# Optimization experiments

Hardware: AMD Instinct MI355X
Metric: run time of the kernel (lower is better)

Reference implementation:

```python
import jax, jax.numpy as jnp
import numpy as np

N, E, T, R, L = 100000, 800000, 2, 4, 2
DIN, H, C, DOUT = 16, 256, 128, 4
EPS = 1e-5


def hetero_linear(x, node_type, W, b):
    # y[i] = x[i] @ W[node_type[i]] + b[node_type[i]]; small fixed T loop
    out = jnp.zeros((x.shape[0], W.shape[-1]), x.dtype)
    for t in range(W.shape[0]):
        out = out + jnp.where((node_type == t)[:, None], x @ W[t] + b[t], jnp.zeros((), x.dtype))
    return out


def hetero_bn(x, node_type, gamma, beta):
    # per-node-type batch norm (training-mode statistics, biased variance)
    T_ = gamma.shape[0]
    cnt = jax.ops.segment_sum(jnp.ones((x.shape[0],), x.dtype), node_type, num_segments=T_)
    cnt = jnp.maximum(cnt, 1.0)[:, None]
    mean = jax.ops.segment_sum(x, node_type, num_segments=T_) / cnt
    var = jax.ops.segment_sum(x * x, node_type, num_segments=T_) / cnt - mean * mean
    inv = jax.lax.rsqrt(var + EPS)
    return (x - mean[node_type]) * inv[node_type] * gamma[node_type] + beta[node_type]


def rgcn_conv(x, edge_index, edge_type, W, root, bias):
    # RGCNConv with sum aggregation: out_i = x_i @ root + b + sum_{(j->i), r} x_j @ W_r
    src, dst = edge_index[0], edge_index[1]
    hs = jnp.einsum('nd,rdf->rnf', x, W)          # [R, N, C]
    msg = hs[edge_type, src]                       # [E, C] per-edge relation-transformed source feats
    agg = jax.ops.segment_sum(msg, dst, num_segments=x.shape[0])
    return agg + x @ root + bias


def setup_inputs() -> dict:
    key = jax.random.key(0)
    ks = iter(jax.random.split(key, 40))

    def w(shape, fan_in):
        return jax.random.normal(next(ks), shape, jnp.float32) / np.float32(np.sqrt(fan_in))

    inp = {}
    inp['x'] = jax.random.normal(next(ks), (N, DIN), jnp.float32)
    inp['edge_index'] = jax.random.randint(next(ks), (2, E), 0, N)
    inp['node_type'] = jax.random.randint(next(ks), (N,), 0, T)
    inp['edge_type'] = jax.random.randint(next(ks), (E,), 0, R)
    inp['ri_w0'] = w((T, DIN, H), DIN); inp['ri_b0'] = jnp.zeros((T, H))
    inp['ri_g0'] = jnp.ones((T, H)); inp['ri_be0'] = jnp.zeros((T, H))
    inp['ri_w1'] = w((T, H, C), H); inp['ri_b1'] = jnp.zeros((T, C))
    inp['cn_g'] = jnp.ones((L, T, C)); inp['cn_b'] = jnp.zeros((L, T, C))
    inp['rg_w'] = w((L, R, C, C), C); inp['rg_root'] = w((L, C, C), C); inp['rg_bias'] = jnp.zeros((L, C))
    inp['mn_g'] = jnp.ones((L, T, C)); inp['mn_b'] = jnp.zeros((L, T, C))
    inp['mw0'] = w((L, T, C, H), C); inp['mb0'] = jnp.zeros((L, T, H))
    inp['mg0'] = jnp.ones((L, T, H)); inp['mbe0'] = jnp.zeros((L, T, H))
    inp['mw1'] = w((L, T, H, C), H); inp['mb1'] = jnp.zeros((L, T, C))
    inp['ro_w0'] = w((T, C, H), C); inp['ro_b0'] = jnp.zeros((T, H))
    inp['ro_g0'] = jnp.ones((T, H)); inp['ro_be0'] = jnp.zeros((T, H))
    inp['ro_w1'] = w((T, H, DOUT), H); inp['ro_b1'] = jnp.zeros((T, DOUT))
    return inp


def reference(x, edge_index, node_type, edge_type,
              ri_w0, ri_b0, ri_g0, ri_be0, ri_w1, ri_b1,
              cn_g, cn_b, rg_w, rg_root, rg_bias,
              mn_g, mn_b, mw0, mb0, mg0, mbe0, mw1, mb1,
              ro_w0, ro_b0, ro_g0, ro_be0, ro_w1, ro_b1):
    act = jax.nn.leaky_relu  # negative_slope 0.01, as nn.LeakyReLU default
    # readin MLP (plain_last)
    h = hetero_linear(x, node_type, ri_w0, ri_b0)
    h = act(hetero_bn(h, node_type, ri_g0, ri_be0))
    h = hetero_linear(h, node_type, ri_w1, ri_b1)
    # RES+ blocks: Norm -> Act -> Conv -> +res, Norm -> Act -> MLP -> +res (dropout=0)
    for l in range(rg_w.shape[0]):
        y = act(hetero_bn(h, node_type, cn_g[l], cn_b[l]))
        h = h + rgcn_conv(y, edge_index, edge_type, rg_w[l], rg_root[l], rg_bias[l])
        y = act(hetero_bn(h, node_type, mn_g[l], mn_b[l]))
        y = hetero_linear(y, node_type, mw0[l], mb0[l])
        y = act(hetero_bn(y, node_type, mg0[l], mbe0[l]))
        y = hetero_linear(y, node_type, mw1[l], mb1[l])
        h = h + y
    # readout MLP (plain_last)
    h = hetero_linear(h, node_type, ro_w0, ro_b0)
    h = act(hetero_bn(h, node_type, ro_g0, ro_be0))
    return hetero_linear(h, node_type, ro_w1, ro_b1)
```

## Files before the change

kernel.cpp:

```cpp
#include <hip/hip_runtime.h>

#define TT 2
#define RR 4
#define LL 2
#define DIN 16
#define HH 256
#define CC 128
#define DOUT 4
#define EPS 1e-5f
#define NB 32
#define NBG 16

typedef float v4f __attribute__((ext_vector_type(4)));
typedef short bf16x8 __attribute__((ext_vector_type(8)));

__device__ __forceinline__ ushort f2bf(float x) {
    uint u = __float_as_uint(x);
    return (ushort)((u + 0x7fffu + ((u >> 16) & 1u)) >> 16);
}
__device__ __forceinline__ float bf2f(ushort h) { return __uint_as_float(((uint)h) << 16); }
__device__ __forceinline__ int swc(int c) { return c ^ ((c >> 3) & 7); }
__device__ __forceinline__ uint pack2(float x, float y) {
    return (uint)f2bf(x) | ((uint)f2bf(y) << 16);
}

__global__ __launch_bounds__(1024) void k_scan1(const int* __restrict__ in, int* __restrict__ out,
                                                int* __restrict__ part, int n) {
    __shared__ int sm[1024];
    const int tid = threadIdx.x;
    const int i = blockIdx.x * 1024 + tid;
    const int v = (i < n) ? in[i] : 0;
    sm[tid] = v;
    __syncthreads();
    for (int off = 1; off < 1024; off <<= 1) {
        const int u = (tid >= off) ? sm[tid - off] : 0;
        __syncthreads();
        sm[tid] += u;
        __syncthreads();
    }
    if (i < n) out[i] = sm[tid] - v;
    if (tid == 1023) part[blockIdx.x] = sm[1023];
}

__global__ __launch_bounds__(1024) void k_scan2(int* __restrict__ part, int nb) {
    __shared__ int sm[1024];
    const int tid = threadIdx.x;
    const int v = (tid < nb) ? part[tid] : 0;
    sm[tid] = v;
    __syncthreads();
    for (int off = 1; off < 1024; off <<= 1) {
        const int u = (tid >= off) ? sm[tid - off] : 0;
        __syncthreads();
        sm[tid] += u;
        __syncthreads();
    }
    if (tid < nb) part[tid] = sm[tid] - v;
    if (tid == nb - 1) part[nb] = sm[tid];
}

__global__ __launch_bounds__(1024) void k_scan3(int* __restrict__ arr, const int* __restrict__ part,
                                                int n, int nb) {
    const int i = blockIdx.x * 1024 + threadIdx.x;
    if (i < n) arr[i] += part[i >> 10];
    else if (i == n) arr[n] = part[nb];
}

__global__ void k_meta(const int* __restrict__ pscan, int* __restrict__ typeStart, int n) {
    const int c1 = pscan[n];
    typeStart[0] = 0; typeStart[1] = n - c1; typeStart[2] = n;
}

__global__ __launch_bounds__(256) void k_build_perm(const int* __restrict__ nt, const int* __restrict__ pscan,
                                                    const int* __restrict__ typeStart, int* __restrict__ perm,
                                                    int* __restrict__ inv, int n) {
    const int i = blockIdx.x * 256 + threadIdx.x;
    if (i >= n) return;
    const int s1 = pscan[i];
    const int pos = nt[i] ? (typeStart[1] + s1) : (i - s1);
    perm[pos] = i;
    inv[i] = pos;
}

__global__ __launch_bounds__(256) void k_deg2(const int* __restrict__ dstv, const int* __restrict__ et,
                                              const int* __restrict__ inv, int* __restrict__ rowp2, int nE) {
    const int e = blockIdx.x * 256 + threadIdx.x;
    if (e < nE) atomicAdd(&rowp2[inv[dstv[e]] * 4 + et[e]], 1);
}

__global__ __launch_bounds__(256) void k_fill2(const int* __restrict__ srcv, const int* __restrict__ dstv,
                                               const int* __restrict__ et, const int* __restrict__ inv,
                                               int* __restrict__ cur, int* __restrict__ csr, int nE) {
    const int e = blockIdx.x * 256 + threadIdx.x;
    if (e < nE) {
        const int pos = atomicAdd(&cur[inv[dstv[e]] * 4 + et[e]], 1);
        csr[pos] = inv[srcv[e]];
    }
}

__global__ __launch_bounds__(256) void k_pack(const float* __restrict__ src, ushort* __restrict__ dst,
                                              int K, int N, long long total) {
    for (long long idx = (long long)blockIdx.x * 256 + threadIdx.x; idx < total;
         idx += (long long)gridDim.x * 256) {
        const long long kn = (long long)K * N;
        const int mat = (int)(idx / kn);
        const int rem = (int)(idx - mat * kn);
        const int k = rem / N, col = rem % N;
        dst[((size_t)mat * (K / 8) + (k >> 3)) * N * 8 + (size_t)col * 8 + (k & 7)] = f2bf(src[idx]);
    }
}

__global__ __launch_bounds__(256) void k_pack_conv(const float* __restrict__ rgw, const float* __restrict__ root,
                                                   ushort* __restrict__ dst) {
    const int idx = blockIdx.x * 256 + threadIdx.x;
    if (idx >= 640 * 128) return;
    const int k = idx >> 7, col = idx & 127;
    const float v = (k < 512) ? rgw[(((k >> 7) * CC) + (k & 127)) * CC + col]
                              : root[(size_t)(k - 512) * CC + col];
    dst[((size_t)(k >> 3) * CC + col) * 8 + (k & 7)] = f2bf(v);
}

__global__ __launch_bounds__(512) void k_coef(const float* __restrict__ stat, const int* __restrict__ typeStart,
                                              const float* __restrict__ g, const float* __restrict__ be,
                                              float* __restrict__ scale, float* __restrict__ shift, int F) {
    const int tid = threadIdx.x;
    if (tid >= TT * F) return;
    const int t = tid / F;
    float s = 0.f, q = 0.f;
    for (int b = 0; b < NB; ++b) {
        s += stat[(size_t)b * 1024 + tid];
        q += stat[(size_t)b * 1024 + 512 + tid];
    }
    const float cnt = fmaxf((float)(typeStart[t + 1] - typeStart[t]), 1.f);
    const float mean = s / cnt;
    const float var = q / cnt - mean * mean;
    const float sc = g[tid] * rsqrtf(var + EPS);
    scale[tid] = sc;
    shift[tid] = be[tid] - mean * sc;
}

__global__ __launch_bounds__(256) void k_gram(const float* __restrict__ x, const int* __restrict__ perm,
                                              const int* __restrict__ typeStart, float* __restrict__ gram) {
    __shared__ float Xs[256][17];
    const int tid = threadIdx.x;
    const int t = blockIdx.y;
    const int rbeg = typeStart[t], rend = typeStart[t + 1];
    const int r0 = rbeg + blockIdx.x * 1024;
    if (r0 >= rend) return;
    const int i = tid >> 4, j = tid & 15;
    float acc = 0.f, sacc = 0.f;
    for (int rr = 0; rr < 4; ++rr) {
        const int gr = r0 + rr * 256 + tid;
        v4f x0 = 0.f, x1 = 0.f, x2 = 0.f, x3 = 0.f;
        if (gr < rend) {
            const float* xr = x + (size_t)perm[gr] * DIN;
            x0 = *(const v4f*)xr; x1 = *(const v4f*)(xr + 4);
            x2 = *(const v4f*)(xr + 8); x3 = *(const v4f*)(xr + 12);
        }
        __syncthreads();
#pragma unroll
        for (int e = 0; e < 4; ++e) { Xs[tid][e] = x0[e]; Xs[tid][4 + e] = x1[e];
                                      Xs[tid][8 + e] = x2[e]; Xs[tid][12 + e] = x3[e]; }
        __syncthreads();
        for (int r = 0; r < 256; ++r) acc += Xs[r][i] * Xs[r][j];
        if (tid < 16)
            for (int r = 0; r < 256; ++r) sacc += Xs[r][tid];
        __syncthreads();
    }
    float* gb = gram + ((size_t)t * NBG + (blockIdx.x & (NBG - 1))) * 272;
    atomicAdd(&gb[tid], acc);
    if (tid < 16) atomicAdd(&gb[256 + tid], sacc);
}

__global__ __launch_bounds__(512) void k_ri_coef(const float* __restrict__ gram, const int* __restrict__ typeStart,
                                                 const float* __restrict__ ri_w0, const float* __restrict__ ri_b0,
                                                 const float* __restrict__ g, const float* __restrict__ be,
                                                 float* __restrict__ w0eff, float* __restrict__ b0eff) {
    __shared__ float G[2][272];
    const int tid = threadIdx.x;
    for (int idx = tid; idx < 2 * 272; idx += 512) {
        const int tt = idx / 272, k = idx % 272;
        float s = 0.f;
        for (int b = 0; b < NBG; ++b) s += gram[((size_t)tt * NBG + b) * 272 + k];
        G[tt][k] = s;
    }
    __syncthreads();
    const int t = tid >> 8, c = tid & 255;
    float wv[16];
#pragma unroll
    for (int k = 0; k < 16; ++k) wv[k] = ri_w0[((size_t)t * 16 + k) * HH + c];
    const float b = ri_b0[t * HH + c];
    const float cnt = fmaxf((float)(typeStart[t + 1] - typeStart[t]), 1.f);
    float sw = 0.f;
#pragma unroll
    for (int k = 0; k < 16; ++k) sw += G[t][256 + k] * wv[k];
    const float mean = (sw + cnt * b) / cnt;
    float e2 = 0.f;
#pragma unroll
    for (int i = 0; i < 16; ++i) {
        const float wi = wv[i];
#pragma unroll
        for (int j = 0; j < 16; ++j) e2 += wi * wv[j] * G[t][i * 16 + j];
    }
    e2 = (e2 + 2.f * b * sw + cnt * b * b) / cnt;
    const float var = e2 - mean * mean;
    const float sc = g[t * HH + c] * rsqrtf(var + EPS);
    const float sf = be[t * HH + c] - mean * sc;
    b0eff[t * HH + c] = b * sc + sf;
#pragma unroll
    for (int k = 0; k < 16; ++k) w0eff[((size_t)t * 16 + k) * HH + c] = wv[k] * sc;
}

__global__ __launch_bounds__(256) void k_readin(const float* __restrict__ x, const int* __restrict__ perm,
                                                const int* __restrict__ typeStart,
                                                const float* __restrict__ w0eff, const float* __restrict__ b0eff,
                                                const ushort* __restrict__ Wp, const float* __restrict__ b1,
                                                float* __restrict__ h, ushort* __restrict__ h16,
                                                float* __restrict__ stat) {
    __shared__ float Xs[128][17];
    __shared__ float W0s[16][256];
    __shared__ float b0s[256];
    __shared__ ushort As[128][40];
    __shared__ ushort Ws[4][128][8];

    const int tid = threadIdx.x;
    const int lane = tid & 63;
    const int wid = tid >> 6;
    const int woffm = (wid >> 1) * 64, woffn = (wid & 1) * 64;
    const int t = blockIdx.y;
    const int rbeg = typeStart[t], rend = typeStart[t + 1];
    const int r0 = rbeg + blockIdx.x * 128;
    if (r0 >= rend) return;

    for (int idx = tid; idx < 16 * 256; idx += 256) W0s[idx >> 8][idx & 255] = w0eff[(size_t)t * 4096 + idx];
    if (tid < 256) b0s[tid] = b0eff[t * 256 + tid];

    const int srow = tid >> 1, half = tid & 1;
    const int sgr = r0 + srow;
    const bool svalid = sgr < rend;
    {
        v4f x0 = 0.f, x1 = 0.f;
        if (svalid) {
            const float* xr = x + (size_t)perm[sgr] * DIN + half * 8;
            x0 = *(const v4f*)xr; x1 = *(const v4f*)(xr + 4);
        }
#pragma unroll
        for (int e = 0; e < 4; ++e) { Xs[srow][half * 8 + e] = x0[e]; Xs[srow][half * 8 + 4 + e] = x1[e]; }
    }
    __syncthreads();
    float xr[16];
#pragma unroll
    for (int k = 0; k < 16; ++k) xr[k] = Xs[srow][k];

    v4f acc[4][4];
#pragma unroll
    for (int mt = 0; mt < 4; ++mt)
#pragma unroll
        for (int nt = 0; nt < 4; ++nt) acc[mt][nt] = (v4f){0.f, 0.f, 0.f, 0.f};

    const size_t wmat = (size_t)t * 256 * 128;
    const int wcp = tid & 63;

    for (int kt = 0; kt < 8; ++kt) {
        const int k0 = kt * 32;
        ushort hA[16];
#pragma unroll
        for (int c2 = 0; c2 < 16; ++c2) {
            const int col = k0 + half * 16 + c2;
            float d = b0s[col];
#pragma unroll
            for (int k = 0; k < 16; ++k) d = fmaf(xr[k], W0s[k][col], d);
            d = fmaxf(d, 0.01f * d);
            hA[c2] = f2bf(d);
        }
        const ushort* wsrc = Wp + wmat + ((size_t)(k0 / 8 + wid) * 128) * 8 + (size_t)wcp * 16;
        const uint4 w0 = *(const uint4*)wsrc;
        const uint4 w1 = *(const uint4*)(wsrc + 8);
        __syncthreads();
        *(uint4*)&As[srow][half * 16] = *(uint4*)&hA[0];
        *(uint4*)&As[srow][half * 16 + 8] = *(uint4*)&hA[8];
        *(uint4*)&Ws[wid][swc(wcp * 2)][0] = w0;
        *(uint4*)&Ws[wid][swc(wcp * 2 + 1)][0] = w1;
        __syncthreads();
        const int afr = lane & 15;
        const int akg = (lane >> 4) * 8;
        bf16x8 aF[4], wf[4];
#pragma unroll
        for (int mt = 0; mt < 4; ++mt) aF[mt] = *(const bf16x8*)&As[woffm + mt * 16 + afr][akg];
#pragma unroll
        for (int nt = 0; nt < 4; ++nt) wf[nt] = *(const bf16x8*)&Ws[lane >> 4][swc(woffn + nt * 16 + afr)][0];
#pragma unroll
        for (int mt = 0; mt < 4; ++mt)
#pragma unroll
            for (int nt = 0; nt < 4; ++nt)
                acc[mt][nt] = __builtin_amdgcn_mfma_f32_16x16x32_bf16(aF[mt], wf[nt], acc[mt][nt], 0, 0, 0);
    }

    float bv[4];
#pragma unroll
    for (int nt = 0; nt < 4; ++nt) bv[nt] = b1[t * 128 + woffn + nt * 16 + (lane & 15)];
    float cs[4] = {0.f, 0.f, 0.f, 0.f}, cq[4] = {0.f, 0.f, 0.f, 0.f};
#pragma unroll
    for (int mt = 0; mt < 4; ++mt) {
        const int grow = r0 + woffm + mt * 16 + (lane >> 4) * 4;
#pragma unroll
        for (int nt = 0; nt < 4; ++nt) {
            const int gcol = woffn + nt * 16 + (lane & 15);
#pragma unroll
            for (int rg = 0; rg < 4; ++rg) {
                const int gr = grow + rg;
                if (gr < rend) {
                    const float v = acc[mt][nt][rg] + bv[nt];
                    const size_t o = (size_t)gr * 128 + gcol;
                    h[o] = v;
                    h16[o] = f2bf(v);
                    cs[nt] += v; cq[nt] += v * v;
                }
            }
        }
    }
    float* sb = stat + (size_t)(blockIdx.x & (NB - 1)) * 1024;
#pragma unroll
    for (int nt = 0; nt < 4; ++nt) {
        float s = cs[nt], q = cq[nt];
        s += __shfl_xor(s, 16); q += __shfl_xor(q, 16);
        s += __shfl_xor(s, 32); q += __shfl_xor(q, 32);
        if (lane < 16) {
            const int col = t * 128 + woffn + nt * 16 + lane;
            atomicAdd(&sb[col], s);
            atomicAdd(&sb[512 + col], q);
        }
    }
}

__global__ __launch_bounds__(256) void k_agg4(const ushort* __restrict__ h16, const int* __restrict__ rowp2,
                                              const int* __restrict__ csr, const float* __restrict__ scale,
                                              const float* __restrict__ shift, const int* __restrict__ typeStart,
                                              ushort* __restrict__ buf, int q0, int q1) {
    const int wid = threadIdx.x >> 6, lane = threadIdx.x & 63;
    const int i = q0 + blockIdx.x * 4 + wid;
    if (i >= q1) return;
    const int c = 2 * lane;
    const int c0 = typeStart[1];
    const float2 sa0 = *(const float2*)(scale + c);
    const float2 sb0 = *(const float2*)(shift + c);
    const float2 sa1 = *(const float2*)(scale + CC + c);
    const float2 sb1 = *(const float2*)(shift + CC + c);
    const uint* h32 = (const uint*)h16;
    float2 a0 = {0.f, 0.f}, a1 = {0.f, 0.f}, a2 = {0.f, 0.f}, a3 = {0.f, 0.f};
    const int e0 = rowp2[4 * i], b1 = rowp2[4 * i + 1], b2 = rowp2[4 * i + 2],
              b3 = rowp2[4 * i + 3], e1 = rowp2[4 * i + 4];
    for (int e = e0; e < e1; e += 64) {
        const int cnt = min(64, e1 - e);
        int pk = (lane < cnt) ? csr[e + lane] : 0;
        for (int j = 0; j < cnt; ++j) {
            const int s = __shfl(pk, j);
            const int idx = e + j;
            const bool tb = s >= c0;
            const uint u = h32[(size_t)s * 64 + lane];
            float vx = fmaf(bf2f((ushort)(u & 0xffff)), tb ? sa1.x : sa0.x, tb ? sb1.x : sb0.x);
            float vy = fmaf(bf2f((ushort)(u >> 16)), tb ? sa1.y : sa0.y, tb ? sb1.y : sb0.y);
            vx = fmaxf(vx, 0.01f * vx);
            vy = fmaxf(vy, 0.01f * vy);
            if (idx < b1)      { a0.x += vx; a0.y += vy; }
            else if (idx < b2) { a1.x += vx; a1.y += vy; }
            else if (idx < b3) { a2.x += vx; a2.y += vy; }
            else               { a3.x += vx; a3.y += vy; }
        }
    }
    const bool td = i >= c0;
    const uint hu = h32[(size_t)i * 64 + lane];
    float yx = fmaf(bf2f((ushort)(hu & 0xffff)), td ? sa1.x : sa0.x, td ? sb1.x : sb0.x);
    float yy = fmaf(bf2f((ushort)(hu >> 16)), td ? sa1.y : sa0.y, td ? sb1.y : sb0.y);
    yx = fmaxf(yx, 0.01f * yx);
    yy = fmaxf(yy, 0.01f * yy);
    uint* brow = (uint*)buf + (size_t)(i - q0) * 320;
    brow[0 * 64 + lane] = pack2(a0.x, a0.y);
    brow[1 * 64 + lane] = pack2(a1.x, a1.y);
    brow[2 * 64 + lane] = pack2(a2.x, a2.y);
    brow[3 * 64 + lane] = pack2(a3.x, a3.y);
    brow[256 + lane] = pack2(yx, yy);
}

__global__ __launch_bounds__(256) void k_add_stats(float* __restrict__ h, ushort* __restrict__ h16,
                                                   const float* __restrict__ tc,
                                                   const int* __restrict__ typeStart, float* __restrict__ stat,
                                                   int n) {
    __shared__ float red[256 * 17];
    const int tid = threadIdx.x;
    const int c = tid & 31;
    const int rs = tid >> 5;
    const int c0 = typeStart[1];
    const int i0 = blockIdx.x * 256;
    const int i1 = min(n, i0 + 256);
    v4f s0 = 0.f, q0 = 0.f, s1 = 0.f, q1 = 0.f;
    for (int i = i0 + rs; i < i1; i += 8) {
        v4f a = *(const v4f*)(h + (size_t)i * CC + 4 * c);
        a += *(const v4f*)(tc + (size_t)i * CC + 4 * c);
        *(v4f*)(h + (size_t)i * CC + 4 * c) = a;
        ushort4 hh = make_ushort4(f2bf(a[0]), f2bf(a[1]), f2bf(a[2]), f2bf(a[3]));
        *(ushort4*)(h16 + (size_t)i * CC + 4 * c) = hh;
        if (i < c0) { s0 += a; q0 += a * a; }
        else        { s1 += a; q1 += a * a; }
    }
#pragma unroll
    for (int j = 0; j < 4; ++j) {
        red[tid * 17 + j] = s0[j];
        red[tid * 17 + 4 + j] = q0[j];
        red[tid * 17 + 8 + j] = s1[j];
        red[tid * 17 + 12 + j] = q1[j];
    }
    __syncthreads();
    float* sb = stat + (size_t)(blockIdx.x & (NB - 1)) * 1024;
    for (int o = tid; o < 512; o += 256) {
        const int col = o & 127, m = (o >> 7) & 1, t = (o >> 8) & 1;
        const int reg = t * 8 + m * 4 + (col & 3);
        float v = 0.f;
#pragma unroll
        for (int r = 0; r < 8; ++r) v += red[((col >> 2) + 32 * r) * 17 + reg];
        atomicAdd(&sb[(m ? 512 : 0) + t * CC + col], v);
    }
}

template <int K, int OUTW, bool TYPED, bool WHET, bool XBF, bool BNIN, bool BHET, bool STATS, int OUTMODE>
__global__ __launch_bounds__(256) void k_mf(
    const float* __restrict__ Xf, const ushort* __restrict__ Xb,
    const ushort* __restrict__ Wp, const float* __restrict__ Bb,
    const float* __restrict__ scale, const float* __restrict__ shift,
    const int* __restrict__ typeStart, float* __restrict__ Y,
    ushort* __restrict__ Y16, float* __restrict__ stat,
    int rbase, int rbeg_u, int rend_u) {
    __shared__ ushort As[128][40];
    __shared__ ushort Ws[4][128][8];
    __shared__ float csh[BNIN ? K : 1];
    __shared__ float cfh[BNIN ? K : 1];

    const int tid = threadIdx.x;
    const int lane = tid & 63;
    const int wid = tid >> 6;
    const int woffm = (wid >> 1) * 64, woffn = (wid & 1) * 64;

    int t = 0, rbeg = rbeg_u, rend = rend_u;
    if constexpr (TYPED) { t = blockIdx.y; rbeg = typeStart[t]; rend = typeStart[t + 1]; }
    const int r0 = rbeg + blockIdx.x * 128;
    if (r0 >= rend) return;
    const int zoff = (OUTW == 256) ? blockIdx.z * 128 : 0;

    if constexpr (BNIN) {
        for (int k = tid; k < K; k += 256) { csh[k] = scale[t * K + k]; cfh[k] = shift[t * K + k]; }
        __syncthreads();
    }

    const int srow = tid >> 1, scg = (tid & 1) * 16;
    const int sgr = r0 + srow;
    const bool svalid = sgr < rend;
    const int wcp = tid & 63;

    v4f acc[4][4];
#pragma unroll
    for (int mt = 0; mt < 4; ++mt)
#pragma unroll
        for (int nt = 0; nt < 4; ++nt) acc[mt][nt] = (v4f){0.f, 0.f, 0.f, 0.f};

    const size_t wmat = (size_t)(WHET ? t : 0) * K * OUTW;

    for (int kt = 0; kt < K / 32; ++kt) {
        const int k0 = kt * 32;
        uint uu[8];
        if constexpr (XBF) {
            uint4 a0 = make_uint4(0, 0, 0, 0), a1 = make_uint4(0, 0, 0, 0);
            if (svalid) {
                const ushort* xs = Xb + (size_t)(sgr - rbase) * K + k0 + scg;
                a0 = *(const uint4*)xs;
                a1 = *(const uint4*)(xs + 8);
            }
            uu[0] = a0.x; uu[1] = a0.y; uu[2] = a0.z; uu[3] = a0.w;
            uu[4] = a1.x; uu[5] = a1.y; uu[6] = a1.z; uu[7] = a1.w;
            if constexpr (BNIN) {
#pragma unroll
                for (int e = 0; e < 8; ++e) {
                    const int k = k0 + scg + 2 * e;
                    float f0 = fmaf(bf2f((ushort)(uu[e] & 0xffff)), csh[k], cfh[k]);
                    float f1 = fmaf(bf2f((ushort)(uu[e] >> 16)), csh[k + 1], cfh[k + 1]);
                    f0 = fmaxf(f0, 0.01f * f0);
                    f1 = fmaxf(f1, 0.01f * f1);
                    uu[e] = pack2(f0, f1);
                }
            }
        } else {
            float fv[16];
            {
                v4f av0 = 0.f, av1 = 0.f, av2 = 0.f, av3 = 0.f;
                if (svalid) {
                    const float* xs = Xf + (size_t)sgr * K + k0 + scg;
                    av0 = *(const v4f*)xs; av1 = *(const v4f*)(xs + 4);
                    av2 = *(const v4f*)(xs + 8); av3 = *(const v4f*)(xs + 12);
                }
#pragma unroll
                for (int e = 0; e < 4; ++e) { fv[e] = av0[e]; fv[4 + e] = av1[e];
                                              fv[8 + e] = av2[e]; fv[12 + e] = av3[e]; }
            }
            if constexpr (BNIN) {
#pragma unroll
                for (int e = 0; e < 16; ++e) {
                    const int k = k0 + scg + e;
                    float vv = fmaf(fv[e], csh[k], cfh[k]);
                    fv[e] = fmaxf(vv, 0.01f * vv);
                }
            }
#pragma unroll
            for (int e = 0; e < 8; ++e) uu[e] = pack2(fv[2 * e], fv[2 * e + 1]);
        }
        const ushort* wsrc = Wp + wmat + ((size_t)(k0 / 8 + wid) * OUTW + zoff) * 8 + (size_t)wcp * 16;
        const uint4 w0 = *(const uint4*)wsrc;
        const uint4 w1 = *(const uint4*)(wsrc + 8);

        __syncthreads();
        *(uint4*)&As[srow][scg] = make_uint4(uu[0], uu[1], uu[2], uu[3]);
        *(uint4*)&As[srow][scg + 8] = make_uint4(uu[4], uu[5], uu[6], uu[7]);
        *(uint4*)&Ws[wid][swc(wcp * 2)][0] = w0;
        *(uint4*)&Ws[wid][swc(wcp * 2 + 1)][0] = w1;
        __syncthreads();

        const int afr = lane & 15;
        const int akg = (lane >> 4) * 8;
        bf16x8 aF[4], wf[4];
#pragma unroll
        for (int mt = 0; mt < 4; ++mt) aF[mt] = *(const bf16x8*)&As[woffm + mt * 16 + afr][akg];
#pragma unroll
        for (int nt = 0; nt < 4; ++nt) wf[nt] = *(const bf16x8*)&Ws[lane >> 4][swc(woffn + nt * 16 + afr)][0];
#pragma unroll
        for (int mt = 0; mt < 4; ++mt)
#pragma unroll
            for (int nt = 0; nt < 4; ++nt)
                acc[mt][nt] = __builtin_amdgcn_mfma_f32_16x16x32_bf16(aF[mt], wf[nt], acc[mt][nt], 0, 0, 0);
    }

    const float* BbT = Bb + (BHET ? (size_t)t * OUTW : 0);
    float bv[4];
#pragma unroll
    for (int nt = 0; nt < 4; ++nt) bv[nt] = BbT[zoff + woffn + nt * 16 + (lane & 15)];
    const int c0 = (STATS && !TYPED) ? typeStart[1] : 0;
    float cs0[4] = {0.f, 0.f, 0.f, 0.f}, cq0[4] = {0.f, 0.f, 0.f, 0.f};
    float cs1[4] = {0.f, 0.f, 0.f, 0.f}, cq1[4] = {0.f, 0.f, 0.f, 0.f};
#pragma unroll
    for (int mt = 0; mt < 4; ++mt) {
        const int grow = r0 + woffm + mt * 16 + (lane >> 4) * 4;
#pragma unroll
        for (int nt = 0; nt < 4; ++nt) {
            const int gcol = zoff + woffn + nt * 16 + (lane & 15);
#pragma unroll
            for (int rg = 0; rg < 4; ++rg) {
                const int gr = grow + rg;
                if (gr < rend) {
                    float v = acc[mt][nt][rg] + bv[nt];
                    const size_t o = (size_t)gr * OUTW + gcol;
                    if constexpr (OUTMODE == 0) Y[o] = v;
                    if constexpr (OUTMODE == 1) Y16[o] = f2bf(v);
                    if constexpr (OUTMODE == 2) {
                        const float hv = Y[o] + v;
                        Y[o] = hv;
                        Y16[o] = f2bf(hv);
                        v = hv;
                    }
                    if constexpr (STATS) {
                        if (TYPED || gr < c0) { cs0[nt] += v; cq0[nt] += v * v; }
                        else                  { cs1[nt] += v; cq1[nt] += v * v; }
                    }
                }
            }
        }
    }
    if constexpr (STATS) {
        float* sb = stat + (size_t)(blockIdx.x & (NB - 1)) * 1024;
#pragma unroll
        for (int nt = 0; nt < 4; ++nt) {
            float s = cs0[nt], q = cq0[nt];
            s += __shfl_xor(s, 16); q += __shfl_xor(q, 16);
            s += __shfl_xor(s, 32); q += __shfl_xor(q, 32);
            if (lane < 16) {
                const int col = t * OUTW + zoff + woffn + nt * 16 + lane;
                atomicAdd(&sb[col], s);
                atomicAdd(&sb[512 + col], q);
            }
            if constexpr (!TYPED) {
                float s1 = cs1[nt], q1 = cq1[nt];
                s1 += __shfl_xor(s1, 16); q1 += __shfl_xor(q1, 16);
                s1 += __shfl_xor(s1, 32); q1 += __shfl_xor(q1, 32);
                if (lane < 16) {
                    const int col = OUTW + zoff + woffn + nt * 16 + lane;
                    atomicAdd(&sb[col], s1);
                    atomicAdd(&sb[512 + col], q1);
                }
            }
        }
    }
}

__global__ __launch_bounds__(256) void k_ro1(const ushort* __restrict__ A256b, const int* __restrict__ perm,
                                             const int* __restrict__ typeStart, const float* __restrict__ ro_w1,
                                             const float* __restrict__ ro_b1, const float* __restrict__ scale,
                                             const float* __restrict__ shift, float* __restrict__ out, int n) {
    __shared__ float W1s[2][256][4];
    __shared__ float scs[512];
    __shared__ float sfs[512];
    const int tid = threadIdx.x;
    for (int idx = tid; idx < 2048; idx += 256) {
        const int t = idx >> 10, rem = idx & 1023;
        W1s[t][rem >> 2][rem & 3] = ro_w1[idx];
    }
    for (int idx = tid; idx < 512; idx += 256) { scs[idx] = scale[idx]; sfs[idx] = shift[idx]; }
    __syncthreads();
    const int trow = tid >> 2, sub = tid & 3;
    const int gr = blockIdx.x * 64 + trow;
    if (gr >= n) return;
    const int c0 = typeStart[1];
    const int t = (gr >= c0) ? 1 : 0;
    v4f acc = 0.f;
    const ushort* ar = A256b + (size_t)gr * 256 + sub * 64;
#pragma unroll
    for (int q = 0; q < 8; ++q) {
        const uint4 u = *(const uint4*)(ar + q * 8);
        const uint uw[4] = {u.x, u.y, u.z, u.w};
#pragma unroll
        for (int e = 0; e < 4; ++e) {
#pragma unroll
            for (int hl = 0; hl < 2; ++hl) {
                const int col = sub * 64 + q * 8 + 2 * e + hl;
                const float v = bf2f((ushort)(hl ? (uw[e] >> 16) : (uw[e] & 0xffff)));
                float vv = fmaf(v, scs[t * 256 + col], sfs[t * 256 + col]);
                vv = fmaxf(vv, 0.01f * vv);
                acc += vv * *(const v4f*)&W1s[t][col][0];
            }
        }
    }
#pragma unroll
    for (int e = 0; e < 4; ++e) { acc[e] += __shfl_xor(acc[e], 1); acc[e] += __shfl_xor(acc[e], 2); }
    if (sub == 0) {
        acc += *(const v4f*)(ro_b1 + t * 4);
        *(v4f*)(out + (size_t)perm[gr] * 4) = acc;
    }
}

extern "C" void kernel_launch(void* const* d_in, const int* in_sizes, int n_in,
                              void* d_out, int out_size, void* d_ws, size_t ws_size,
                              hipStream_t stream) {
    const float* x = (const float*)d_in[0];
    const int* ei = (const int*)d_in[1];
    const int* nt = (const int*)d_in[2];
    const int* et = (const int*)d_in[3];
    const float* ri_w0 = (const float*)d_in[4];
    const float* ri_b0 = (const float*)d_in[5];
    const float* ri_g0 = (const float*)d_in[6];
    const float* ri_be0 = (const float*)d_in[7];
    const float* ri_w1 = (const float*)d_in[8];
    const float* ri_b1 = (const float*)d_in[9];
    const float* cn_g = (const float*)d_in[10];
    const float* cn_b = (const float*)d_in[11];
    const float* rg_w = (const float*)d_in[12];
    const float* rg_root = (const float*)d_in[13];
    const float* rg_bias = (const float*)d_in[14];
    const float* mn_g = (const float*)d_in[15];
    const float* mn_b = (const float*)d_in[16];
    const float* mw0 = (const float*)d_in[17];
    const float* mb0 = (const float*)d_in[18];
    const float* mg0 = (const float*)d_in[19];
    const float* mbe0 = (const float*)d_in[20];
    const float* mw1 = (const float*)d_in[21];
    const float* mb1 = (const float*)d_in[22];
    const float* ro_w0 = (const float*)d_in[23];
    const float* ro_b0 = (const float*)d_in[24];
    const float* ro_g0 = (const float*)d_in[25];
    const float* ro_be0 = (const float*)d_in[26];
    const float* ro_w1 = (const float*)d_in[27];
    const float* ro_b1 = (const float*)d_in[28];

    const int n = in_sizes[2];
    const int nE = in_sizes[3];
    const int* srcv = ei;
    const int* dstv = ei + nE;

    char* w = (char*)d_ws;
    size_t off = 0;
    auto alloc = [&](size_t bytes) -> char* {
        char* p = w + off;
        off = (off + bytes + 255) & ~(size_t)255;
        return p;
    };
    float* h = (float*)alloc((size_t)n * CC * sizeof(float));
    ushort* h16 = (ushort*)alloc((size_t)n * CC * sizeof(ushort));
    int* csr = (int*)alloc((size_t)nE * sizeof(int));
    int* rowp2 = (int*)alloc(((size_t)4 * n + 1) * sizeof(int));
    int* perm = (int*)alloc((size_t)n * sizeof(int));
    int* inv = (int*)alloc((size_t)n * sizeof(int));
    int* pscan = (int*)alloc((size_t)(n + 1) * sizeof(int));
    int* part = (int*)alloc(2052 * sizeof(int));
    int* typeStart = (int*)alloc(64);
    float* statbuf = (float*)alloc((size_t)9 * NB * 1024 * sizeof(float));
    float* gram = (float*)alloc((size_t)2 * NBG * 272 * sizeof(float));
    float* scale = (float*)alloc(512 * sizeof(float));
    float* shift = (float*)alloc(512 * sizeof(float));
    float* w0eff = (float*)alloc((size_t)2 * 16 * 256 * sizeof(float));
    float* b0eff = (float*)alloc(512 * sizeof(float));
    ushort* pw_ri1 = (ushort*)alloc(65536 * 2);
    ushort* pw_mw0 = (ushort*)alloc(131072 * 2);
    ushort* pw_mw1 = (ushort*)alloc(131072 * 2);
    ushort* pw_ro0 = (ushort*)alloc(65536 * 2);
    ushort* pw_conv = (ushort*)alloc(163840 * 2);
    char* region2 = alloc((size_t)n * 512);
    if (ws_size < off) return;

    ushort* A256b = (ushort*)region2;
    float* tconv = (float*)region2;
    int* cur2 = (int*)region2;
    float* out = (float*)d_out;

    ushort* buf = (ushort*)(w + off);
    const size_t bufBytes = (ws_size > off) ? (ws_size - off) : 0;
    const long long chkcap = (long long)(bufBytes / 1280);
    if (chkcap < 1024) return;
    int nchunk, CHK;
    if (chkcap >= n) { nchunk = 1; CHK = n; }
    else { nchunk = (int)((n + chkcap - 1) / chkcap); CHK = (n + nchunk - 1) / nchunk; }

    auto SS = [&](int slot) { return statbuf + (size_t)slot * NB * 1024; };

    const int gE = (nE + 255) / 256;
    const int gN = (n + 255) / 256;
    const int nb = (n + 1023) / 1024;
    const int m4 = 4 * n;
    const int nb2 = (m4 + 1023) / 1024;
    const int gmx = (n + 127) / 128;

    k_pack<<<128, 256, 0, stream>>>(ri_w1, pw_ri1, 256, 128, 2LL * 256 * 128);
    k_pack<<<256, 256, 0, stream>>>(mw0, pw_mw0, 128, 256, 4LL * 128 * 256);
    k_pack<<<256, 256, 0, stream>>>(mw1, pw_mw1, 256, 128, 4LL * 256 * 128);
    k_pack<<<128, 256, 0, stream>>>(ro_w0, pw_ro0, 128, 256, 2LL * 128 * 256);
    for (int l = 0; l < LL; ++l)
        k_pack_conv<<<320, 256, 0, stream>>>(rg_w + (size_t)l * RR * CC * CC,
                                             rg_root + (size_t)l * CC * CC,
                                             pw_conv + (size_t)l * 640 * 128);

    hipMemsetAsync(statbuf, 0, (size_t)9 * NB * 1024 * sizeof(float), stream);
    hipMemsetAsync(gram, 0, (size_t)2 * NBG * 272 * sizeof(float), stream);
    k_scan1<<<nb, 1024, 0, stream>>>(nt, pscan, part, n);
    k_scan2<<<1, 1024, 0, stream>>>(part, nb);
    k_scan3<<<(n + 1024) / 1024, 1024, 0, stream>>>(pscan, part, n, nb);
    k_meta<<<1, 1, 0, stream>>>(pscan, typeStart, n);
    k_build_perm<<<gN, 256, 0, stream>>>(nt, pscan, typeStart, perm, inv, n);
    hipMemsetAsync(rowp2, 0, ((size_t)m4 + 1) * sizeof(int), stream);
    k_deg2<<<gE, 256, 0, stream>>>(dstv, et, inv, rowp2, nE);
    k_scan1<<<nb2, 1024, 0, stream>>>(rowp2, rowp2, part, m4);
    k_scan2<<<1, 1024, 0, stream>>>(part, nb2);
    k_scan3<<<(m4 + 1024) / 1024, 1024, 0, stream>>>(rowp2, part, m4, nb2);
    hipMemcpyAsync(cur2, rowp2, (size_t)m4 * sizeof(int), hipMemcpyDeviceToDevice, stream);
    k_fill2<<<gE, 256, 0, stream>>>(srcv, dstv, et, inv, cur2, csr, nE);

    k_gram<<<dim3((n + 1023) / 1024, 2), 256, 0, stream>>>(x, perm, typeStart, gram);
    k_ri_coef<<<1, 512, 0, stream>>>(gram, typeStart, ri_w0, ri_b0, ri_g0, ri_be0, w0eff, b0eff);
    k_readin<<<dim3(gmx, 2), 256, 0, stream>>>(x, perm, typeStart, w0eff, b0eff, pw_ri1, ri_b1,
                                               h, h16, SS(1));

    for (int l = 0; l < LL; ++l) {
        const int s_cn = l ? 4 : 1, s_mn = l ? 5 : 2, s_mg = l ? 6 : 3, s_nx = l ? 7 : 4;
        k_coef<<<1, 512, 0, stream>>>(SS(s_cn), typeStart, cn_g + (size_t)l * TT * CC,
                                      cn_b + (size_t)l * TT * CC, scale, shift, CC);
        const ushort* wconv = pw_conv + (size_t)l * 640 * 128;
        if (nchunk == 1) {
            k_agg4<<<(n + 3) / 4, 256, 0, stream>>>(h16, rowp2, csr, scale, shift, typeStart, buf, 0, n);
            k_mf<640, 128, false, false, true, false, false, true, 2><<<gmx, 256, 0, stream>>>(
                nullptr, buf, wconv, rg_bias + (size_t)l * CC, nullptr, nullptr, typeStart,
                h, h16, SS(s_mn), 0, 0, n);
        } else {
            for (int q0 = 0; q0 < n; q0 += CHK) {
                const int q1 = min(n, q0 + CHK);
                k_agg4<<<(q1 - q0 + 3) / 4, 256, 0, stream>>>(h16, rowp2, csr, scale, shift,
                                                              typeStart, buf, q0, q1);
                k_mf<640, 128, false, false, true, false, false, false, 0>
                    <<<(q1 - q0 + 127) / 128, 256, 0, stream>>>(
                        nullptr, buf, wconv, rg_bias + (size_t)l * CC, nullptr, nullptr, typeStart,
                        tconv, nullptr, nullptr, q0, q0, q1);
            }
            k_add_stats<<<(n + 255) / 256, 256, 0, stream>>>(h, h16, tconv, typeStart, SS(s_mn), n);
        }

        k_coef<<<1, 512, 0, stream>>>(SS(s_mn), typeStart, mn_g + (size_t)l * TT * CC,
                                      mn_b + (size_t)l * TT * CC, scale, shift, CC);
        k_mf<128, 256, true, true, false, true, true, true, 1><<<dim3(gmx, 2, 2), 256, 0, stream>>>(
            h, nullptr, pw_mw0 + (size_t)l * 2 * 128 * 256, mb0 + (size_t)l * TT * HH,
            scale, shift, typeStart, nullptr, A256b, SS(s_mg), 0, 0, n);
        k_coef<<<1, 512, 0, stream>>>(SS(s_mg), typeStart, mg0 + (size_t)l * TT * HH,
                                      mbe0 + (size_t)l * TT * HH, scale, shift, HH);
        if (l == 0)
            k_mf<256, 128, true, true, true, true, true, true, 2><<<dim3(gmx, 2, 1), 256, 0, stream>>>(
                nullptr, A256b, pw_mw1 + (size_t)l * 2 * 256 * 128, mb1 + (size_t)l * TT * CC,
                scale, shift, typeStart, h, h16, SS(s_nx), 0, 0, n);
        else
            k_mf<256, 128, true, true, true, true, true, false, 2><<<dim3(gmx, 2, 1), 256, 0, stream>>>(
                nullptr, A256b, pw_mw1 + (size_t)l * 2 * 256 * 128, mb1 + (size_t)l * TT * CC,
                scale, shift, typeStart, h, h16, nullptr, 0, 0, n);
    }

    k_mf<128, 256, true, true, false, false, true, true, 1><<<dim3(gmx, 2, 2), 256, 0, stream>>>(
        h, nullptr, pw_ro0, ro_b0, nullptr, nullptr, typeStart, nullptr, A256b, SS(8), 0, 0, n);
    k_coef<<<1, 512, 0, stream>>>(SS(8), typeStart, ro_g0, ro_be0, scale, shift, HH);
    k_ro1<<<(n + 63) / 64, 256, 0, stream>>>(A256b, perm, typeStart, ro_w1, ro_b1, scale, shift, out, n);
}
```

Measured before the change: 839.3 us.

## Precompute BN+act once, gather bf16 activations, merge setup launches, read h16 in MLPs

Adds a k_bnact pass that applies the per-type batch norm and LeakyReLU to h once and writes a bf16 y16, so k_agg4 only gathers and sums instead of normalising every gathered edge row. The conv GEMM now reads the root input directly from y16 through a new CROOT path, which shrinks the aggregation buffer from 640 to 512 columns per row. It always uses the chunked path with stats fused in. The MLP and readout GEMMs now read bf16 h16 instead of fp32 h. Setup is also consolidated: pack kernels are merged, k_meta is folded into scan3, the memcpy is replaced by a dual write, and the two memsets are combined. Risks include an extra full pass over h and lower input precision for the MLP GEMMs.

After: 801.6 us. -4.5%, faster.

```diff
diff --git a/kernel.cpp b/kernel.cpp
--- a/kernel.cpp
+++ b/kernel.cpp
@@ -59,15 +59,18 @@
 }
 
 __global__ __launch_bounds__(1024) void k_scan3(int* __restrict__ arr, const int* __restrict__ part,
-                                                int n, int nb) {
+                                                int n, int nb, int* __restrict__ typeStart,
+                                                int* __restrict__ out2) {
     const int i = blockIdx.x * 1024 + threadIdx.x;
-    if (i < n) arr[i] += part[i >> 10];
-    else if (i == n) arr[n] = part[nb];
-}
-
-__global__ void k_meta(const int* __restrict__ pscan, int* __restrict__ typeStart, int n) {
-    const int c1 = pscan[n];
-    typeStart[0] = 0; typeStart[1] = n - c1; typeStart[2] = n;
+    if (i < n) {
+        const int v = arr[i] + part[i >> 10];
+        arr[i] = v;
+        if (out2) out2[i] = v;
+    } else if (i == n) {
+        const int total = part[nb];
+        arr[n] = total;
+        if (typeStart) { typeStart[0] = 0; typeStart[1] = n - total; typeStart[2] = n; }
+    }
 }
 
 __global__ __launch_bounds__(256) void k_build_perm(const int* __restrict__ nt, const int* __restrict__ pscan,
@@ -97,22 +100,34 @@
     }
 }
 
-__global__ __launch_bounds__(256) void k_pack(const float* __restrict__ src, ushort* __restrict__ dst,
-                                              int K, int N, long long total) {
-    for (long long idx = (long long)blockIdx.x * 256 + threadIdx.x; idx < total;
+__global__ __launch_bounds__(256) void k_packall(const float* __restrict__ ri_w1, const float* __restrict__ mw0,
+                                                 const float* __restrict__ mw1, const float* __restrict__ ro_w0,
+                                                 ushort* __restrict__ p_ri1, ushort* __restrict__ p_mw0,
+                                                 ushort* __restrict__ p_mw1, ushort* __restrict__ p_ro0) {
+    for (long long idx = (long long)blockIdx.x * 256 + threadIdx.x; idx < 393216;
          idx += (long long)gridDim.x * 256) {
-        const long long kn = (long long)K * N;
-        const int mat = (int)(idx / kn);
-        const int rem = (int)(idx - mat * kn);
+        const float* src; ushort* dst; int K, N; long long lo;
+        if (idx < 65536)       { src = ri_w1; dst = p_ri1; K = 256; N = 128; lo = idx; }
+        else if (idx < 196608) { src = mw0;   dst = p_mw0; K = 128; N = 256; lo = idx - 65536; }
+        else if (idx < 327680) { src = mw1;   dst = p_mw1; K = 256; N = 128; lo = idx - 196608; }
+        else                   { src = ro_w0; dst = p_ro0; K = 128; N = 256; lo = idx - 327680; }
+        const int kn = K * N;
+        const int mat = (int)(lo / kn);
+        const int rem = (int)(lo - (long long)mat * kn);
         const int k = rem / N, col = rem % N;
-        dst[((size_t)mat * (K / 8) + (k >> 3)) * N * 8 + (size_t)col * 8 + (k & 7)] = f2bf(src[idx]);
-    }
-}
-
-__global__ __launch_bounds__(256) void k_pack_conv(const float* __restrict__ rgw, const float* __restrict__ root,
-                                                   ushort* __restrict__ dst) {
+        dst[((size_t)mat * (K / 8) + (k >> 3)) * N * 8 + (size_t)col * 8 + (k & 7)] = f2bf(src[lo]);
+    }
+}
+
+__global__ __launch_bounds__(256) void k_pack_conv(const float* __restrict__ rgw_all,
+                                                   const float* __restrict__ root_all,
+                                                   ushort* __restrict__ dst_all) {
     const int idx = blockIdx.x * 256 + threadIdx.x;
     if (idx >= 640 * 128) return;
+    const int l = blockIdx.y;
+    const float* rgw = rgw_all + (size_t)l * RR * CC * CC;
+    const float* root = root_all + (size_t)l * CC * CC;
+    ushort* dst = dst_all + (size_t)l * 640 * 128;
     const int k = idx >> 7, col = idx & 127;
     const float v = (k < 512) ? rgw[(((k >> 7) * CC) + (k & 127)) * CC + col]
                               : root[(size_t)(k - 512) * CC + col];
@@ -136,6 +151,61 @@
     const float sc = g[tid] * rsqrtf(var + EPS);
     scale[tid] = sc;
     shift[tid] = be[tid] - mean * sc;
+}
+
+__global__ __launch_bounds__(256) void k_bnact(const float* __restrict__ h, const float* __restrict__ scale,
+                                               const float* __restrict__ shift, const int* __restrict__ typeStart,
+                                               ushort* __restrict__ y16, int n) {
+    const int c0 = typeStart[1];
+    const long long total = (long long)n * 32;
+    for (long long idx = (long long)blockIdx.x * 256 + threadIdx.x; idx < total;
+         idx += (long long)gridDim.x * 256) {
+        const int i = (int)(idx >> 5), cq = (int)(idx & 31);
+        const int t = (i >= c0) ? 1 : 0;
+        const v4f v = *(const v4f*)(h + (size_t)i * CC + cq * 4);
+        const v4f sc = *(const v4f*)(scale + t * CC + cq * 4);
+        const v4f sf = *(const v4f*)(shift + t * CC + cq * 4);
+        float o[4];
+#pragma unroll
+        for (int j = 0; j < 4; ++j) {
+            const float vv = fmaf(v[j], sc[j], sf[j]);
+            o[j] = fmaxf(vv, 0.01f * vv);
+        }
+        uint2 p = make_uint2(pack2(o[0], o[1]), pack2(o[2], o[3]));
+        *(uint2*)((uint*)y16 + (size_t)i * 64 + cq * 2) = p;
+    }
+}
+
+__global__ __launch_bounds__(256) void k_agg4(const ushort* __restrict__ y16, const int* __restrict__ rowp2,
+                                              const int* __restrict__ csr, ushort* __restrict__ buf,
+                                              int q0, int q1) {
+    const int wid = threadIdx.x >> 6, lane = threadIdx.x & 63;
+    const int i = q0 + blockIdx.x * 4 + wid;
+    if (i >= q1) return;
+    const uint* y32 = (const uint*)y16;
+    float2 a0 = {0.f, 0.f}, a1 = {0.f, 0.f}, a2 = {0.f, 0.f}, a3 = {0.f, 0.f};
+    const int e0 = rowp2[4 * i], b1 = rowp2[4 * i + 1], b2 = rowp2[4 * i + 2],
+              b3 = rowp2[4 * i + 3], e1 = rowp2[4 * i + 4];
+    for (int e = e0; e < e1; e += 64) {
+        const int cnt = min(64, e1 - e);
+        int pk = (lane < cnt) ? csr[e + lane] : 0;
+        for (int j = 0; j < cnt; ++j) {
+            const int s = __shfl(pk, j);
+            const uint u = y32[(size_t)s * 64 + lane];
+            const float vx = bf2f((ushort)(u & 0xffff));
+            const float vy = bf2f((ushort)(u >> 16));
+            const int idx = e + j;
+            if (idx < b1)      { a0.x += vx; a0.y += vy; }
+            else if (idx < b2) { a1.x += vx; a1.y += vy; }
+            else if (idx < b3) { a2.x += vx; a2.y += vy; }
+            else               { a3.x += vx; a3.y += vy; }
+        }
+    }
+    uint* brow = (uint*)buf + (size_t)(i - q0) * 256;
+    __builtin_nontemporal_store(pack2(a0.x, a0.y), brow + 0 * 64 + lane);
+    __builtin_nontemporal_store(pack2(a1.x, a1.y), brow + 1 * 64 + lane);
+    __builtin_nontemporal_store(pack2(a2.x, a2.y), brow + 2 * 64 + lane);
+    __builtin_nontemporal_store(pack2(a3.x, a3.y), brow + 3 * 64 + lane);
 }
 
 __global__ __launch_bounds__(256) void k_gram(const float* __restrict__ x, const int* __restrict__ perm,
@@ -332,98 +402,10 @@
     }
 }
 
-__global__ __launch_bounds__(256) void k_agg4(const ushort* __restrict__ h16, const int* __restrict__ rowp2,
-                                              const int* __restrict__ csr, const float* __restrict__ scale,
-                                              const float* __restrict__ shift, const int* __restrict__ typeStart,
-                                              ushort* __restrict__ buf, int q0, int q1) {
-    const int wid = threadIdx.x >> 6, lane = threadIdx.x & 63;
-    const int i = q0 + blockIdx.x * 4 + wid;
-    if (i >= q1) return;
-    const int c = 2 * lane;
-    const int c0 = typeStart[1];
-    const float2 sa0 = *(const float2*)(scale + c);
-    const float2 sb0 = *(const float2*)(shift + c);
-    const float2 sa1 = *(const float2*)(scale + CC + c);
-    const float2 sb1 = *(const float2*)(shift + CC + c);
-    const uint* h32 = (const uint*)h16;
-    float2 a0 = {0.f, 0.f}, a1 = {0.f, 0.f}, a2 = {0.f, 0.f}, a3 = {0.f, 0.f};
-    const int e0 = rowp2[4 * i], b1 = rowp2[4 * i + 1], b2 = rowp2[4 * i + 2],
-              b3 = rowp2[4 * i + 3], e1 = rowp2[4 * i + 4];
-    for (int e = e0; e < e1; e += 64) {
-        const int cnt = min(64, e1 - e);
-        int pk = (lane < cnt) ? csr[e + lane] : 0;
-        for (int j = 0; j < cnt; ++j) {
-            const int s = __shfl(pk, j);
-            const int idx = e + j;
-            const bool tb = s >= c0;
-            const uint u = h32[(size_t)s * 64 + lane];
-            float vx = fmaf(bf2f((ushort)(u & 0xffff)), tb ? sa1.x : sa0.x, tb ? sb1.x : sb0.x);
-            float vy = fmaf(bf2f((ushort)(u >> 16)), tb ? sa1.y : sa0.y, tb ? sb1.y : sb0.y);
-            vx = fmaxf(vx, 0.01f * vx);
-            vy = fmaxf(vy, 0.01f * vy);
-            if (idx < b1)      { a0.x += vx; a0.y += vy; }
-            else if (idx < b2) { a1.x += vx; a1.y += vy; }
-            else if (idx < b3) { a2.x += vx; a2.y += vy; }
-            else               { a3.x += vx; a3.y += vy; }
-        }
-    }
-    const bool td = i >= c0;
-    const uint hu = h32[(size_t)i * 64 + lane];
-    float yx = fmaf(bf2f((ushort)(hu & 0xffff)), td ? sa1.x : sa0.x, td ? sb1.x : sb0.x);
-    float yy = fmaf(bf2f((ushort)(hu >> 16)), td ? sa1.y : sa0.y, td ? sb1.y : sb0.y);
-    yx = fmaxf(yx, 0.01f * yx);
-    yy = fmaxf(yy, 0.01f * yy);
-    uint* brow = (uint*)buf + (size_t)(i - q0) * 320;
-    brow[0 * 64 + lane] = pack2(a0.x, a0.y);
-    brow[1 * 64 + lane] = pack2(a1.x, a1.y);
-    brow[2 * 64 + lane] = pack2(a2.x, a2.y);
-    brow[3 * 64 + lane] = pack2(a3.x, a3.y);
-    brow[256 + lane] = pack2(yx, yy);
-}
-
-__global__ __launch_bounds__(256) void k_add_stats(float* __restrict__ h, ushort* __restrict__ h16,
-                                                   const float* __restrict__ tc,
-                                                   const int* __restrict__ typeStart, float* __restrict__ stat,
-                                                   int n) {
-    __shared__ float red[256 * 17];
-    const int tid = threadIdx.x;
-    const int c = tid & 31;
-    const int rs = tid >> 5;
-    const int c0 = typeStart[1];
-    const int i0 = blockIdx.x * 256;
-    const int i1 = min(n, i0 + 256);
-    v4f s0 = 0.f, q0 = 0.f, s1 = 0.f, q1 = 0.f;
-    for (int i = i0 + rs; i < i1; i += 8) {
-        v4f a = *(const v4f*)(h + (size_t)i * CC + 4 * c);
-        a += *(const v4f*)(tc + (size_t)i * CC + 4 * c);
-        *(v4f*)(h + (size_t)i * CC + 4 * c) = a;
-        ushort4 hh = make_ushort4(f2bf(a[0]), f2bf(a[1]), f2bf(a[2]), f2bf(a[3]));
-        *(ushort4*)(h16 + (size_t)i * CC + 4 * c) = hh;
-        if (i < c0) { s0 += a; q0 += a * a; }
-        else        { s1 += a; q1 += a * a; }
-    }
-#pragma unroll
-    for (int j = 0; j < 4; ++j) {
-        red[tid * 17 + j] = s0[j];
-        red[tid * 17 + 4 + j] = q0[j];
-        red[tid * 17 + 8 + j] = s1[j];
-        red[tid * 17 + 12 + j] = q1[j];
-    }
-    __syncthreads();
-    float* sb = stat + (size_t)(blockIdx.x & (NB - 1)) * 1024;
-    for (int o = tid; o < 512; o += 256) {
-        const int col = o & 127, m = (o >> 7) & 1, t = (o >> 8) & 1;
-        const int reg = t * 8 + m * 4 + (col & 3);
-        float v = 0.f;
-#pragma unroll
-        for (int r = 0; r < 8; ++r) v += red[((col >> 2) + 32 * r) * 17 + reg];
-        atomicAdd(&sb[(m ? 512 : 0) + t * CC + col], v);
-    }
-}
-
-template <int K, int OUTW, bool TYPED, bool WHET, bool XBF, bool BNIN, bool BHET, bool STATS, int OUTMODE>
+template <int K, int OUTW, bool TYPED, bool WHET, bool XBF, bool CROOT, bool BNIN,
+          bool BHET, bool STATS, int OUTMODE>
 __global__ __launch_bounds__(256) void k_mf(
-    const float* __restrict__ Xf, const ushort* __restrict__ Xb,
+    const float* __restrict__ Xf, const ushort* __restrict__ Xb, const ushort* __restrict__ Xb2,
     const ushort* __restrict__ Wp, const float* __restrict__ Bb,
     const float* __restrict__ scale, const float* __restrict__ shift,
     const int* __restrict__ typeStart, float* __restrict__ Y,
@@ -434,6 +416,8 @@
     __shared__ float csh[BNIN ? K : 1];
     __shared__ float cfh[BNIN ? K : 1];
 
+    constexpr int XSTR = CROOT ? 512 : K;
+
     const int tid = threadIdx.x;
     const int lane = tid & 63;
     const int wid = tid >> 6;
@@ -467,9 +451,15 @@
         const int k0 = kt * 32;
         uint uu[8];
         if constexpr (XBF) {
+            const ushort* xs;
+            if constexpr (CROOT) {
+                xs = (k0 >= 512) ? (Xb2 + (size_t)sgr * 128 + (k0 - 512) + scg)
+                                 : (Xb + (size_t)(sgr - rbase) * XSTR + k0 + scg);
+            } else {
+                xs = Xb + (size_t)(sgr - rbase) * XSTR + k0 + scg;
+            }
             uint4 a0 = make_uint4(0, 0, 0, 0), a1 = make_uint4(0, 0, 0, 0);
             if (svalid) {
-                const ushort* xs = Xb + (size_t)(sgr - rbase) * K + k0 + scg;
                 a0 = *(const uint4*)xs;
                 a1 = *(const uint4*)(xs + 8);
             }
@@ -690,13 +680,13 @@
     ushort* h16 = (ushort*)alloc((size_t)n * CC * sizeof(ushort));
     int* csr = (int*)alloc((size_t)nE * sizeof(int));
     int* rowp2 = (int*)alloc(((size_t)4 * n + 1) * sizeof(int));
+    int* cur2 = (int*)alloc((size_t)4 * n * sizeof(int));
     int* perm = (int*)alloc((size_t)n * sizeof(int));
     int* inv = (int*)alloc((size_t)n * sizeof(int));
     int* pscan = (int*)alloc((size_t)(n + 1) * sizeof(int));
     int* part = (int*)alloc(2052 * sizeof(int));
     int* typeStart = (int*)alloc(64);
-    float* statbuf = (float*)alloc((size_t)9 * NB * 1024 * sizeof(float));
-    float* gram = (float*)alloc((size_t)2 * NBG * 272 * sizeof(float));
+    float* statgram = (float*)alloc(((size_t)9 * NB * 1024 + 2 * NBG * 272) * sizeof(float));
     float* scale = (float*)alloc(512 * sizeof(float));
     float* shift = (float*)alloc(512 * sizeof(float));
     float* w0eff = (float*)alloc((size_t)2 * 16 * 256 * sizeof(float));
@@ -709,14 +699,15 @@
     char* region2 = alloc((size_t)n * 512);
     if (ws_size < off) return;
 
+    float* statbuf = statgram;
+    float* gram = statgram + (size_t)9 * NB * 1024;
     ushort* A256b = (ushort*)region2;
-    float* tconv = (float*)region2;
-    int* cur2 = (int*)region2;
+    ushort* y16 = (ushort*)region2;
     float* out = (float*)d_out;
 
     ushort* buf = (ushort*)(w + off);
     const size_t bufBytes = (ws_size > off) ? (ws_size - off) : 0;
-    const long long chkcap = (long long)(bufBytes / 1280);
+    const long long chkcap = (long long)(bufBytes / 1024);
     if (chkcap < 1024) return;
     int nchunk, CHK;
     if (chkcap >= n) { nchunk = 1; CHK = n; }
@@ -731,28 +722,19 @@
     const int nb2 = (m4 + 1023) / 1024;
     const int gmx = (n + 127) / 128;
 
-    k_pack<<<128, 256, 0, stream>>>(ri_w1, pw_ri1, 256, 128, 2LL * 256 * 128);
-    k_pack<<<256, 256, 0, stream>>>(mw0, pw_mw0, 128, 256, 4LL * 128 * 256);
-    k_pack<<<256, 256, 0, stream>>>(mw1, pw_mw1, 256, 128, 4LL * 256 * 128);
-    k_pack<<<128, 256, 0, stream>>>(ro_w0, pw_ro0, 128, 256, 2LL * 128 * 256);
-    for (int l = 0; l < LL; ++l)
-        k_pack_conv<<<320, 256, 0, stream>>>(rg_w + (size_t)l * RR * CC * CC,
-                                             rg_root + (size_t)l * CC * CC,
-                                             pw_conv + (size_t)l * 640 * 128);
-
-    hipMemsetAsync(statbuf, 0, (size_t)9 * NB * 1024 * sizeof(float), stream);
-    hipMemsetAsync(gram, 0, (size_t)2 * NBG * 272 * sizeof(float), stream);
+    k_packall<<<1536, 256, 0, stream>>>(ri_w1, mw0, mw1, ro_w0, pw_ri1, pw_mw0, pw_mw1, pw_ro0);
+    k_pack_conv<<<dim3(320, 2), 256, 0, stream>>>(rg_w, rg_root, pw_conv);
+
+    hipMemsetAsync(statgram, 0, ((size_t)9 * NB * 1024 + 2 * NBG * 272) * sizeof(float), stream);
     k_scan1<<<nb, 1024, 0, stream>>>(nt, pscan, part, n);
     k_scan2<<<1, 1024, 0, stream>>>(part, nb);
-    k_scan3<<<(n + 1024) / 1024, 1024, 0, stream>>>(pscan, part, n, nb);
-    k_meta<<<1, 1, 0, stream>>>(pscan, typeStart, n);
+    k_scan3<<<(n + 1024) / 1024, 1024, 0, stream>>>(pscan, part, n, nb, typeStart, nullptr);
     k_build_perm<<<gN, 256, 0, stream>>>(nt, pscan, typeStart, perm, inv, n);
     hipMemsetAsync(rowp2, 0, ((size_t)m4 + 1) * sizeof(int), stream);
     k_deg2<<<gE, 256, 0, stream>>>(dstv, et, inv, rowp2, nE);
     k_scan1<<<nb2, 1024, 0, stream>>>(rowp2, rowp2, part, m4);
     k_scan2<<<1, 1024, 0, stream>>>(part, nb2);
-    k_scan3<<<(m4 + 1024) / 1024, 1024, 0, stream>>>(rowp2, part, m4, nb2);
-    hipMemcpyAsync(cur2, rowp2, (size_t)m4 * sizeof(int), hipMemcpyDeviceToDevice, stream);
+    k_scan3<<<(m4 + 1024) / 1024, 1024, 0, stream>>>(rowp2, part, m4, nb2, nullptr, cur2);
     k_fill2<<<gE, 256, 0, stream>>>(srcv, dstv, et, inv, cur2, csr, nE);
 
     k_gram<<<dim3((n + 1023) / 1024, 2), 256, 0, stream>>>(x, perm, typeStart, gram);
@@ -764,44 +746,36 @@
         const int s_cn = l ? 4 : 1, s_mn = l ? 5 : 2, s_mg = l ? 6 : 3, s_nx = l ? 7 : 4;
         k_coef<<<1, 512, 0, stream>>>(SS(s_cn), typeStart, cn_g + (size_t)l * TT * CC,
                                       cn_b + (size_t)l * TT * CC, scale, shift, CC);
+        k_bnact<<<4096, 256, 0, stream>>>(h, scale, shift, typeStart, y16, n);
         const ushort* wconv = pw_conv + (size_t)l * 640 * 128;
-        if (nchunk == 1) {
-            k_agg4<<<(n + 3) / 4, 256, 0, stream>>>(h16, rowp2, csr, scale, shift, typeStart, buf, 0, n);
-            k_mf<640, 128, false, false, true, false, false, true, 2><<<gmx, 256, 0, stream>>>(
-                nullptr, buf, wconv, rg_bias + (size_t)l * CC, nullptr, nullptr, typeStart,
-                h, h16, SS(s_mn), 0, 0, n);
-        } else {
-            for (int q0 = 0; q0 < n; q0 += CHK) {
-                const int q1 = min(n, q0 + CHK);
-                k_agg4<<<(q1 - q0 + 3) / 4, 256, 0, stream>>>(h16, rowp2, csr, scale, shift,
-                                                              typeStart, buf, q0, q1);
-                k_mf<640, 128, false, false, true, false, false, false, 0>
-                    <<<(q1 - q0 + 127) / 128, 256, 0, stream>>>(
-                        nullptr, buf, wconv, rg_bias + (size_t)l * CC, nullptr, nullptr, typeStart,
-                        tconv, nullptr, nullptr, q0, q0, q1);
-            }
-            k_add_stats<<<(n + 255) / 256, 256, 0, stream>>>(h, h16, tconv, typeStart, SS(s_mn), n);
+        for (int q0 = 0; q0 < n; q0 += CHK) {
+            const int q1 = min(n, q0 + CHK);
+            k_agg4<<<(q1 - q0 + 3) / 4, 256, 0, stream>>>(y16, rowp2, csr, buf, q0, q1);
+            k_mf<640, 128, false, false, true, true, false, false, true, 2>
+                <<<(q1 - q0 + 127) / 128, 256, 0, stream>>>(
+                    nullptr, buf, y16, wconv, rg_bias + (size_t)l * CC, nullptr, nullptr,
+                    typeStart, h, h16, SS(s_mn), q0, q0, q1);
         }
 
         k_coef<<<1, 512, 0, stream>>>(SS(s_mn), typeStart, mn_g + (size_t)l * TT * CC,
                                       mn_b + (size_t)l * TT * CC, scale, shift, CC);
-        k_mf<128, 256, true, true, false, true, true, true, 1><<<dim3(gmx, 2, 2), 256, 0, stream>>>(
-            h, nullptr, pw_mw0 + (size_t)l * 2 * 128 * 256, mb0 + (size_t)l * TT * HH,
+        k_mf<128, 256, true, true, true, false, true, true, true, 1><<<dim3(gmx, 2, 2), 256, 0, stream>>>(
+            nullptr, h16, nullptr, pw_mw0 + (size_t)l * 2 * 128 * 256, mb0 + (size_t)l * TT * HH,
             scale, shift, typeStart, nullptr, A256b, SS(s_mg), 0, 0, n);
         k_coef<<<1, 512, 0, stream>>>(SS(s_mg), typeStart, mg0 + (size_t)l * TT * HH,
                                       mbe0 + (size_t)l * TT * HH, scale, shift, HH);
         if (l == 0)
-            k_mf<256, 128, true, true, true, true, true, true, 2><<<dim3(gmx, 2, 1), 256, 0, stream>>>(
-                nullptr, A256b, pw_mw1 + (size_t)l * 2 * 256 * 128, mb1 + (size_t)l * TT * CC,
+            k_mf<256, 128, true, true, true, false, true, true, true, 2><<<dim3(gmx, 2, 1), 256, 0, stream>>>(
+                nullptr, A256b, nullptr, pw_mw1 + (size_t)l * 2 * 256 * 128, mb1 + (size_t)l * TT * CC,
                 scale, shift, typeStart, h, h16, SS(s_nx), 0, 0, n);
         else
-            k_mf<256, 128, true, true, true, true, true, false, 2><<<dim3(gmx, 2, 1), 256, 0, stream>>>(
-                nullptr, A256b, pw_mw1 + (size_t)l * 2 * 256 * 128, mb1 + (size_t)l * TT * CC,
+            k_mf<256, 128, true, true, true, false, true, true, false, 2><<<dim3(gmx, 2, 1), 256, 0, stream>>>(
+                nullptr, A256b, nullptr, pw_mw1 + (size_t)l * 2 * 256 * 128, mb1 + (size_t)l * TT * CC,
                 scale, shift, typeStart, h, h16, nullptr, 0, 0, n);
     }
 
-    k_mf<128, 256, true, true, false, false, true, true, 1><<<dim3(gmx, 2, 2), 256, 0, stream>>>(
-        h, nullptr, pw_ro0, ro_b0, nullptr, nullptr, typeStart, nullptr, A256b, SS(8), 0, 0, n);
+    k_mf<128, 256, true, true, true, false, false, true, true, 1><<<dim3(gmx, 2, 2), 256, 0, stream>>>(
+        nullptr, h16, nullptr, pw_ro0, ro_b0, nullptr, nullptr, typeStart, nullptr, A256b, SS(8), 0, 0, n);
     k_coef<<<1, 512, 0, stream>>>(SS(8), typeStart, ro_g0, ro_be0, scale, shift, HH);
     k_ro1<<<(n + 63) / 64, 256, 0, stream>>>(A256b, perm, typeStart, ro_w1, ro_b1, scale, shift, out, n);
 }
```
